# Kernel tuning notes

Hardware: AMD Instinct MI355X
Metric: run time of the kernel (lower is better)

The kernel has to match this reference:

```python
import jax, jax.numpy as jnp
import numpy as np

# PointPillars KITTI config (from init_kwargs)
VOXEL_SIZE = np.array([0.16, 0.16, 4.0], dtype=np.float32)
PC_LO = np.array([0.0, -39.68, -3.0], dtype=np.float32)
PC_HI = np.array([69.12, 39.68, 1.0], dtype=np.float32)
GRID = np.round((PC_HI - PC_LO) / VOXEL_SIZE).astype(np.int32)  # [432, 496, 1]
MAX_PTS = 32
MAX_VOX = 40000  # forward uses max_voxels[1]
B, N, C = 4, 120000, 4


def _voxelize_one(pts):
    """Hard-voxelize one point cloud. pts: (N, C) float32.
    Returns padded (MAX_VOX, MAX_PTS, C) voxels, (MAX_VOX, 3) int32 coords
    (x,y,z; -1 for padding slots), (MAX_VOX,) int32 point counts (0 = padding).
    Voxels are ordered by first occurrence in point order, and points within a
    voxel are filled in point order (first MAX_PTS), matching hard_voxelize_cpu."""
    grid = jnp.asarray(GRID)
    lo = jnp.asarray(PC_LO)
    hi = jnp.asarray(PC_HI)
    vs = jnp.asarray(VOXEL_SIZE)

    xyz = pts[:, :3]
    inb = jnp.all((xyz >= lo) & (xyz < hi), axis=1)                       # (N,)
    coords = jnp.clip(jnp.floor((xyz - lo) / vs).astype(jnp.int32), 0, grid - 1)
    flat = coords[:, 0] * (grid[1] * grid[2]) + coords[:, 1] * grid[2] + coords[:, 2]
    SENT = jnp.int32(int(GRID[0]) * int(GRID[1]) * int(GRID[2]))
    flat = jnp.where(inb, flat, SENT)                                     # out-of-range -> sentinel bin

    # stable sort groups equal flat-ids while preserving point order
    order_s = jnp.argsort(flat, stable=True)                              # (N,)
    fs = flat[order_s]
    is_first = jnp.concatenate([jnp.ones((1,), bool), fs[1:] != fs[:-1]])
    gid_s = jnp.cumsum(is_first.astype(jnp.int32)) - 1                    # group id per sorted pos

    # per-group stats (num_segments = N covers worst case; empty segs -> int max)
    first_pt = jax.ops.segment_min(order_s.astype(jnp.int32), gid_s, num_segments=N)
    group_flat = jax.ops.segment_min(fs, gid_s, num_segments=N)
    cnt_g = jax.ops.segment_sum(jnp.ones((N,), jnp.int32), gid_s, num_segments=N)
    valid_g = group_flat < SENT

    # slot = rank of first occurrence among valid groups (np.argsort(first_idx))
    key = jnp.where(valid_g, first_pt, jnp.int32(N))
    g_order = jnp.argsort(key)
    slot_of_group = jnp.zeros((N,), jnp.int32).at[g_order].set(jnp.arange(N, dtype=jnp.int32))

    # per-point group / slot / within-voxel rank (rank = order of arrival)
    pgid = jnp.zeros((N,), jnp.int32).at[order_s].set(gid_s)
    pslot = slot_of_group[pgid]
    start_s = jax.ops.segment_min(jnp.arange(N, dtype=jnp.int32), gid_s, num_segments=N)
    wrank_s = jnp.arange(N, dtype=jnp.int32) - start_s[gid_s]
    wrank = jnp.zeros((N,), jnp.int32).at[order_s].set(wrank_s)

    pvalid = inb & (pslot < MAX_VOX) & (wrank < MAX_PTS)
    tslot = jnp.where(pvalid, pslot, jnp.int32(MAX_VOX))                  # dump invalid into pad row
    trank = jnp.where(pvalid, wrank, 0)
    voxels = jnp.zeros((MAX_VOX + 1, MAX_PTS, C), pts.dtype).at[tslot, trank].set(pts)[:MAX_VOX]

    gslot = jnp.where(valid_g & (slot_of_group < MAX_VOX), slot_of_group, jnp.int32(MAX_VOX))
    gcoords = coords[jnp.clip(first_pt, 0, N - 1)]
    out_coords = jnp.full((MAX_VOX + 1, 3), -1, jnp.int32).at[gslot].set(gcoords)[:MAX_VOX]
    npts = jnp.zeros((MAX_VOX + 1,), jnp.int32).at[gslot].set(jnp.minimum(cnt_g, MAX_PTS))[:MAX_VOX]
    return voxels, out_coords, npts


def setup_inputs() -> dict:
    key = jax.random.key(0)
    k1, k2 = jax.random.split(key)
    # xyz uniform slightly beyond the pc_range so some points are filtered out
    lo = jnp.array([-2.0, -42.0, -3.2], jnp.float32)
    hi = jnp.array([71.0, 42.0, 1.2], jnp.float32)
    xyz = lo + jax.random.uniform(k1, (B, N, 3), jnp.float32) * (hi - lo)
    inten = jax.random.uniform(k2, (B, N, 1), jnp.float32)
    return {"points": jnp.concatenate([xyz, inten], axis=-1)}


def reference(points):
    voxels, coords, npts = jax.vmap(_voxelize_one)(points)                # (B, MAX_VOX, ...)
    pillars = voxels.reshape(B * MAX_VOX, MAX_PTS, C)
    batch_idx = jnp.broadcast_to(jnp.arange(B, dtype=jnp.int32)[:, None, None], (B, MAX_VOX, 1))
    # padding slots (npts == 0) keep batch idx -1 like their -1 coords
    batch_idx = jnp.where(npts[..., None] > 0, batch_idx, -1)
    coors_batch = jnp.concatenate([batch_idx, coords], axis=-1).reshape(B * MAX_VOX, 4)
    npoints = npts.reshape(B * MAX_VOX)
    return pillars, coors_batch, npoints
```

## Files before the change

### kernel.cpp

```cpp
#include <hip/hip_runtime.h>
#include <stdint.h>

#define BB      4
#define NPTS    120000
#define GX      432
#define GY      496
#define GG      (GX*GY)
#define MAXVOX  40000
#define MAXP    32
#define CHUNK   512
#define NCH     235
#define NBLK    (BB*NCH)
#define NT      (NBLK*256)

#define OFF_COOR 20480000
#define OFF_NPTS 21120000

#define POISON    0xAAAAAAAAu
#define SPIN_CAP  (1u<<22)
#define AGENT __HIP_MEMORY_SCOPE_AGENT


__device__ __forceinline__ unsigned aload(const unsigned* p) {
    return __hip_atomic_load(p, __ATOMIC_RELAXED, AGENT);
}
__device__ __forceinline__ void astore(unsigned* p, unsigned v) {
    __hip_atomic_store(p, v, __ATOMIC_RELAXED, AGENT);
}

__device__ __forceinline__ int compute_flat(float4 pt) {
    float x = pt.x, y = pt.y, z = pt.z;
    bool inb = (x >= 0.0f) && (x < 69.12f) &&
               (y >= -39.68f) && (y < 39.68f) &&
               (z >= -3.0f) && (z < 1.0f);
    if (!inb) return -1;
    int cx = (int)floorf((x - 0.0f) / 0.16f);
    int cy = (int)floorf((y + 39.68f) / 0.16f);
    cx = min(max(cx, 0), GX - 1);
    cy = min(max(cy, 0), GY - 1);
    return cx * GY + cy;
}

__global__ __launch_bounds__(256) void k1z(const float* __restrict__ pts,
        unsigned int* __restrict__ head, unsigned int* __restrict__ nxt,
        float* __restrict__ out)
{
    const int tid = threadIdx.x, blk = blockIdx.x;
    const int b = blk / NCH, c = blk - b * NCH;
    const int base = c * CHUNK;
    const float4* pp = (const float4*)pts + (size_t)b * NPTS;
    const int p0 = base + tid, p1 = base + 256 + tid;
    int f0 = -1, f1 = -1;
    if (p0 < NPTS) f0 = compute_flat(pp[p0]);
    if (p1 < NPTS) f1 = compute_flat(pp[p1]);
    if (f0 >= 0)
        nxt[b * NPTS + p0] = atomicExch(&head[b * GG + f0], (unsigned)p0);
    if (f1 >= 0)
        nxt[b * NPTS + p1] = atomicExch(&head[b * GG + f1], (unsigned)p1);

    const int gt = blk * 256 + tid;
    const float4 z = make_float4(0.f, 0.f, 0.f, 0.f);
    float4* o4 = (float4*)out;
    for (int i = gt; i < 5120000; i += NT) o4[i] = z;
    const float4 neg1 = make_float4(-1.f, -1.f, -1.f, -1.f);
    float4* c4 = (float4*)(out + OFF_COOR);
    if (gt < 160000) c4[gt] = neg1;
    float4* n4 = (float4*)(out + OFF_NPTS);
    if (gt < 40000) n4[gt] = z;
}

__global__ __launch_bounds__(256) void k2w(const float* __restrict__ pts,
        const unsigned int* __restrict__ head, const unsigned int* __restrict__ nxt,
        unsigned int* __restrict__ descr, float* __restrict__ out)
{
    const int tid = threadIdx.x, blk = blockIdx.x;
    const int b = blk / NCH, c = blk - b * NCH;
    const int base = c * CHUNK;
    const int lane = tid & 63, wv = tid >> 6;
    const int p0 = base + tid, p1 = base + 256 + tid;
    const float4* pp = (const float4*)pts + (size_t)b * NPTS;
    const unsigned* nx = nxt + (size_t)b * NPTS;

    int f0 = -1, f1 = -1;
    if (p0 < NPTS) f0 = compute_flat(pp[p0]);
    if (p1 < NPTS) f1 = compute_flat(pp[p1]);
    unsigned hd0 = 0, hd1 = 0, mn0 = 0xFFFFFFFFu, mn1 = 0xFFFFFFFFu;
    int cnt0 = 0, cnt1 = 0;
    if (f0 >= 0) {
        hd0 = head[b * GG + f0];
        for (unsigned node = hd0; node != POISON; node = nx[node]) {
            ++cnt0; mn0 = min(mn0, node);
        }
    }
    if (f1 >= 0) {
        hd1 = head[b * GG + f1];
        for (unsigned node = hd1; node != POISON; node = nx[node]) {
            ++cnt1; mn1 = min(mn1, node);
        }
    }
    int flag0 = (f0 >= 0 && mn0 == (unsigned)p0);
    int flag1 = (f1 >= 0 && mn1 == (unsigned)p1);

    unsigned long long mA = __ballot(flag0);
    unsigned long long mB = __ballot(flag1);
    __shared__ int wsA[4], wsB[4];
    __shared__ int s_excl;
    if (lane == 0) { wsA[wv] = __popcll(mA); wsB[wv] = __popcll(mB); }
    __syncthreads();
    int preA = 0, preB = 0, totA = 0, totB = 0;
    #pragma unroll
    for (int i = 0; i < 4; ++i) {
        if (i < wv) { preA += wsA[i]; preB += wsB[i]; }
        totA += wsA[i]; totB += wsB[i];
    }
    unsigned long long below = (1ull << lane) - 1ull;
    int rank0 = preA + __popcll(mA & below);
    int rank1 = totA + preB + __popcll(mB & below);
    int total = totA + totB;

    if (tid == 0 && c > 0)
        astore(&descr[blk], 0x40000000u | (unsigned)total);

    if (wv == 0) {
        int excl = 0, pos = c;
        while (pos > 0) {
            int w = min(64, pos);
            int st = 0, val = 0;
            if (lane < w) {
                const unsigned* src = &descr[b * NCH + (pos - 1 - lane)];
                unsigned word; unsigned it = 0;
                do { word = aload(src); st = (int)(word >> 30); }
                while (!(st & 1) && ++it < SPIN_CAP);
                val = (int)(word & 0x3FFFFFFFu);
            }
            unsigned long long pmask = __ballot(st == 3);
            int contrib;
            if (pmask) {
                int j = (int)(__ffsll((long long)pmask) - 1);
                contrib = (lane <= j) ? val : 0;
                pos = 0;
            } else {
                contrib = (lane < w) ? val : 0;
                pos -= w;
            }
            #pragma unroll
            for (int off = 1; off < 64; off <<= 1)
                contrib += __shfl_xor(contrib, off, 64);
            excl += contrib;
        }
        if (lane == 0) {
            s_excl = excl;
            astore(&descr[blk], 0xC0000000u | (unsigned)(excl + total));
        }
    }
    __syncthreads();
    int excl = s_excl;

    #pragma unroll
    for (int h = 0; h < 2; ++h) {
        int flg = h ? flag1 : flag0;
        if (!flg) continue;
        int f = h ? f1 : f0;
        int s = excl + (h ? rank1 : rank0);
        if (s >= MAXVOX) continue;
        unsigned hd = h ? hd1 : hd0;
        int cnt = h ? cnt1 : cnt0;
        int t = b * MAXVOX + s;
        int m = min(cnt, MAXP);
        float4* prow = (float4*)out + (size_t)t * MAXP;
        int prev = -1;
        for (int r = 0; r < m; ++r) {
            int cur = 0x7FFFFFFF;
            for (unsigned node = hd; node != POISON; node = nx[node]) {
                int pi = (int)node;
                if (pi > prev && pi < cur) cur = pi;
            }
            prow[r] = pp[cur];
            prev = cur;
        }
        float* coor = out + (size_t)OFF_COOR + (size_t)t * 4;
        coor[0] = (float)b;
        coor[1] = (float)(f / GY);
        coor[2] = (float)(f % GY);
        coor[3] = 0.f;
        out[OFF_NPTS + t] = (float)m;
    }
}

extern "C" void kernel_launch(void* const* d_in, const int* in_sizes, int n_in,
                              void* d_out, int out_size, void* d_ws, size_t ws_size,
                              hipStream_t stream) {
    const float* pts = (const float*)d_in[0];
    float* out = (float*)d_out;

    auto align256 = [](size_t x) { return (x + 255) & ~(size_t)255; };
    char* w = (char*)d_ws;
    unsigned int* head  = (unsigned int*)w; w += align256((size_t)BB * GG * 4);
    unsigned int* nxt   = (unsigned int*)w; w += align256((size_t)BB * NPTS * 4);
    unsigned int* descr = (unsigned int*)w; w += align256((size_t)NBLK * 4);

    k1z<<<NBLK, 256, 0, stream>>>(pts, head, nxt, out);
    k2w<<<NBLK, 256, 0, stream>>>(pts, head, nxt, descr, out);
}
```

Before: 136.9 us.

## Fuse linking and compaction kernels via cooperative grid sync, early-exit chain walk

```diff
diff --git a/kernel.cpp b/kernel.cpp
--- a/kernel.cpp
+++ b/kernel.cpp
@@ -1,4 +1,5 @@
 #include <hip/hip_runtime.h>
+#include <hip/hip_cooperative_groups.h>
 #include <stdint.h>
 
 #define BB      4
@@ -20,6 +21,8 @@
 #define SPIN_CAP  (1u<<22)
 #define AGENT __HIP_MEMORY_SCOPE_AGENT
 
+namespace cg = cooperative_groups;
+
 
 __device__ __forceinline__ unsigned aload(const unsigned* p) {
     return __hip_atomic_load(p, __ATOMIC_RELAXED, AGENT);
@@ -41,22 +44,25 @@
     return cx * GY + cy;
 }
 
-__global__ __launch_bounds__(256) void k1z(const float* __restrict__ pts,
+__global__ __launch_bounds__(256, 4) void kf(const float* __restrict__ pts,
         unsigned int* __restrict__ head, unsigned int* __restrict__ nxt,
-        float* __restrict__ out)
+        unsigned int* __restrict__ descr, float* __restrict__ out)
 {
     const int tid = threadIdx.x, blk = blockIdx.x;
     const int b = blk / NCH, c = blk - b * NCH;
     const int base = c * CHUNK;
+    const int lane = tid & 63, wv = tid >> 6;
+    const int p0 = base + tid, p1 = base + 256 + tid;
     const float4* pp = (const float4*)pts + (size_t)b * NPTS;
-    const int p0 = base + tid, p1 = base + 256 + tid;
+    unsigned* nx = nxt + (size_t)b * NPTS;
+
     int f0 = -1, f1 = -1;
     if (p0 < NPTS) f0 = compute_flat(pp[p0]);
     if (p1 < NPTS) f1 = compute_flat(pp[p1]);
     if (f0 >= 0)
-        nxt[b * NPTS + p0] = atomicExch(&head[b * GG + f0], (unsigned)p0);
+        nx[p0] = atomicExch(&head[b * GG + f0], (unsigned)p0);
     if (f1 >= 0)
-        nxt[b * NPTS + p1] = atomicExch(&head[b * GG + f1], (unsigned)p1);
+        nx[p1] = atomicExch(&head[b * GG + f1], (unsigned)p1);
 
     const int gt = blk * 256 + tid;
     const float4 z = make_float4(0.f, 0.f, 0.f, 0.f);
@@ -67,39 +73,30 @@
     if (gt < 160000) c4[gt] = neg1;
     float4* n4 = (float4*)(out + OFF_NPTS);
     if (gt < 40000) n4[gt] = z;
-}
-
-__global__ __launch_bounds__(256) void k2w(const float* __restrict__ pts,
-        const unsigned int* __restrict__ head, const unsigned int* __restrict__ nxt,
-        unsigned int* __restrict__ descr, float* __restrict__ out)
-{
-    const int tid = threadIdx.x, blk = blockIdx.x;
-    const int b = blk / NCH, c = blk - b * NCH;
-    const int base = c * CHUNK;
-    const int lane = tid & 63, wv = tid >> 6;
-    const int p0 = base + tid, p1 = base + 256 + tid;
-    const float4* pp = (const float4*)pts + (size_t)b * NPTS;
-    const unsigned* nx = nxt + (size_t)b * NPTS;
-
-    int f0 = -1, f1 = -1;
-    if (p0 < NPTS) f0 = compute_flat(pp[p0]);
-    if (p1 < NPTS) f1 = compute_flat(pp[p1]);
-    unsigned hd0 = 0, hd1 = 0, mn0 = 0xFFFFFFFFu, mn1 = 0xFFFFFFFFu;
+
+    __builtin_amdgcn_fence(__ATOMIC_RELEASE, "agent");
+    cg::this_grid().sync();
+    __builtin_amdgcn_fence(__ATOMIC_ACQUIRE, "agent");
+
+    unsigned hd0 = 0, hd1 = 0;
     int cnt0 = 0, cnt1 = 0;
+    int flag0 = 0, flag1 = 0;
     if (f0 >= 0) {
         hd0 = head[b * GG + f0];
+        flag0 = 1;
         for (unsigned node = hd0; node != POISON; node = nx[node]) {
-            ++cnt0; mn0 = min(mn0, node);
+            ++cnt0;
+            if ((int)node < p0) { flag0 = 0; break; }
         }
     }
     if (f1 >= 0) {
         hd1 = head[b * GG + f1];
+        flag1 = 1;
         for (unsigned node = hd1; node != POISON; node = nx[node]) {
-            ++cnt1; mn1 = min(mn1, node);
-        }
-    }
-    int flag0 = (f0 >= 0 && mn0 == (unsigned)p0);
-    int flag1 = (f1 >= 0 && mn1 == (unsigned)p1);
+            ++cnt1;
+            if ((int)node < p1) { flag1 = 0; break; }
+        }
+    }
 
     unsigned long long mA = __ballot(flag0);
     unsigned long long mB = __ballot(flag1);
@@ -187,6 +184,150 @@
     }
 }
 
+__global__ __launch_bounds__(256) void k1z(const float* __restrict__ pts,
+        unsigned int* __restrict__ head, unsigned int* __restrict__ nxt,
+        float* __restrict__ out)
+{
+    const int tid = threadIdx.x, blk = blockIdx.x;
+    const int b = blk / NCH, c = blk - b * NCH;
+    const int base = c * CHUNK;
+    const float4* pp = (const float4*)pts + (size_t)b * NPTS;
+    const int p0 = base + tid, p1 = base + 256 + tid;
+    int f0 = -1, f1 = -1;
+    if (p0 < NPTS) f0 = compute_flat(pp[p0]);
+    if (p1 < NPTS) f1 = compute_flat(pp[p1]);
+    if (f0 >= 0)
+        nxt[b * NPTS + p0] = atomicExch(&head[b * GG + f0], (unsigned)p0);
+    if (f1 >= 0)
+        nxt[b * NPTS + p1] = atomicExch(&head[b * GG + f1], (unsigned)p1);
+
+    const int gt = blk * 256 + tid;
+    const float4 z = make_float4(0.f, 0.f, 0.f, 0.f);
+    float4* o4 = (float4*)out;
+    for (int i = gt; i < 5120000; i += NT) o4[i] = z;
+    const float4 neg1 = make_float4(-1.f, -1.f, -1.f, -1.f);
+    float4* c4 = (float4*)(out + OFF_COOR);
+    if (gt < 160000) c4[gt] = neg1;
+    float4* n4 = (float4*)(out + OFF_NPTS);
+    if (gt < 40000) n4[gt] = z;
+}
+
+__global__ __launch_bounds__(256) void k2w(const float* __restrict__ pts,
+        const unsigned int* __restrict__ head, const unsigned int* __restrict__ nxt,
+        unsigned int* __restrict__ descr, float* __restrict__ out)
+{
+    const int tid = threadIdx.x, blk = blockIdx.x;
+    const int b = blk / NCH, c = blk - b * NCH;
+    const int base = c * CHUNK;
+    const int lane = tid & 63, wv = tid >> 6;
+    const int p0 = base + tid, p1 = base + 256 + tid;
+    const float4* pp = (const float4*)pts + (size_t)b * NPTS;
+    const unsigned* nx = nxt + (size_t)b * NPTS;
+
+    int f0 = -1, f1 = -1;
+    if (p0 < NPTS) f0 = compute_flat(pp[p0]);
+    if (p1 < NPTS) f1 = compute_flat(pp[p1]);
+    unsigned hd0 = 0, hd1 = 0;
+    int cnt0 = 0, cnt1 = 0, flag0 = 0, flag1 = 0;
+    if (f0 >= 0) {
+        hd0 = head[b * GG + f0]; flag0 = 1;
+        for (unsigned node = hd0; node != POISON; node = nx[node]) {
+            ++cnt0; if ((int)node < p0) { flag0 = 0; break; }
+        }
+    }
+    if (f1 >= 0) {
+        hd1 = head[b * GG + f1]; flag1 = 1;
+        for (unsigned node = hd1; node != POISON; node = nx[node]) {
+            ++cnt1; if ((int)node < p1) { flag1 = 0; break; }
+        }
+    }
+
+    unsigned long long mA = __ballot(flag0);
+    unsigned long long mB = __ballot(flag1);
+    __shared__ int wsA[4], wsB[4];
+    __shared__ int s_excl;
+    if (lane == 0) { wsA[wv] = __popcll(mA); wsB[wv] = __popcll(mB); }
+    __syncthreads();
+    int preA = 0, preB = 0, totA = 0, totB = 0;
+    #pragma unroll
+    for (int i = 0; i < 4; ++i) {
+        if (i < wv) { preA += wsA[i]; preB += wsB[i]; }
+        totA += wsA[i]; totB += wsB[i];
+    }
+    unsigned long long below = (1ull << lane) - 1ull;
+    int rank0 = preA + __popcll(mA & below);
+    int rank1 = totA + preB + __popcll(mB & below);
+    int total = totA + totB;
+
+    if (tid == 0 && c > 0)
+        astore(&descr[blk], 0x40000000u | (unsigned)total);
+
+    if (wv == 0) {
+        int excl = 0, pos = c;
+        while (pos > 0) {
+            int w = min(64, pos);
+            int st = 0, val = 0;
+            if (lane < w) {
+                const unsigned* src = &descr[b * NCH + (pos - 1 - lane)];
+                unsigned word; unsigned it = 0;
+                do { word = aload(src); st = (int)(word >> 30); }
+                while (!(st & 1) && ++it < SPIN_CAP);
+                val = (int)(word & 0x3FFFFFFFu);
+            }
+            unsigned long long pmask = __ballot(st == 3);
+            int contrib;
+            if (pmask) {
+                int j = (int)(__ffsll((long long)pmask) - 1);
+                contrib = (lane <= j) ? val : 0;
+                pos = 0;
+            } else {
+                contrib = (lane < w) ? val : 0;
+                pos -= w;
+            }
+            #pragma unroll
+            for (int off = 1; off < 64; off <<= 1)
+                contrib += __shfl_xor(contrib, off, 64);
+            excl += contrib;
+        }
+        if (lane == 0) {
+            s_excl = excl;
+            astore(&descr[blk], 0xC0000000u | (unsigned)(excl + total));
+        }
+    }
+    __syncthreads();
+    int excl = s_excl;
+
+    #pragma unroll
+    for (int h = 0; h < 2; ++h) {
+        int flg = h ? flag1 : flag0;
+        if (!flg) continue;
+        int f = h ? f1 : f0;
+        int s = excl + (h ? rank1 : rank0);
+        if (s >= MAXVOX) continue;
+        unsigned hd = h ? hd1 : hd0;
+        int cnt = h ? cnt1 : cnt0;
+        int t = b * MAXVOX + s;
+        int m = min(cnt, MAXP);
+        float4* prow = (float4*)out + (size_t)t * MAXP;
+        int prev = -1;
+        for (int r = 0; r < m; ++r) {
+            int cur = 0x7FFFFFFF;
+            for (unsigned node = hd; node != POISON; node = nx[node]) {
+                int pi = (int)node;
+                if (pi > prev && pi < cur) cur = pi;
+            }
+            prow[r] = pp[cur];
+            prev = cur;
+        }
+        float* coor = out + (size_t)OFF_COOR + (size_t)t * 4;
+        coor[0] = (float)b;
+        coor[1] = (float)(f / GY);
+        coor[2] = (float)(f % GY);
+        coor[3] = 0.f;
+        out[OFF_NPTS + t] = (float)m;
+    }
+}
+
 extern "C" void kernel_launch(void* const* d_in, const int* in_sizes, int n_in,
                               void* d_out, int out_size, void* d_ws, size_t ws_size,
                               hipStream_t stream) {
@@ -199,6 +340,12 @@
     unsigned int* nxt   = (unsigned int*)w; w += align256((size_t)BB * NPTS * 4);
     unsigned int* descr = (unsigned int*)w; w += align256((size_t)NBLK * 4);
 
-    k1z<<<NBLK, 256, 0, stream>>>(pts, head, nxt, out);
-    k2w<<<NBLK, 256, 0, stream>>>(pts, head, nxt, descr, out);
-}
+    void* args[] = { (void*)&pts, (void*)&head, (void*)&nxt,
+                     (void*)&descr, (void*)&out };
+    hipError_t e = hipLaunchCooperativeKernel(reinterpret_cast<void*>(kf),
+                       dim3(NBLK), dim3(256), args, 0, stream);
+    if (e != hipSuccess) {
+        k1z<<<NBLK, 256, 0, stream>>>(pts, head, nxt, out);
+        k2w<<<NBLK, 256, 0, stream>>>(pts, head, nxt, descr, out);
+    }
+}
```

Result: slower. 369.3 us (+169.7%).

## Drop full output zero-fill; pad only unused rows and tail slots

Applied to the files above, without the earlier changes.

```diff
diff --git a/kernel.cpp b/kernel.cpp
--- a/kernel.cpp
+++ b/kernel.cpp
@@ -21,6 +21,7 @@
 #define AGENT __HIP_MEMORY_SCOPE_AGENT
 
 
+
 __device__ __forceinline__ unsigned aload(const unsigned* p) {
     return __hip_atomic_load(p, __ATOMIC_RELAXED, AGENT);
 }
@@ -41,9 +42,8 @@
     return cx * GY + cy;
 }
 
-__global__ __launch_bounds__(256) void k1z(const float* __restrict__ pts,
-        unsigned int* __restrict__ head, unsigned int* __restrict__ nxt,
-        float* __restrict__ out)
+__global__ __launch_bounds__(256) void k1a(const float* __restrict__ pts,
+        unsigned int* __restrict__ head, unsigned int* __restrict__ nxt)
 {
     const int tid = threadIdx.x, blk = blockIdx.x;
     const int b = blk / NCH, c = blk - b * NCH;
@@ -57,19 +57,9 @@
         nxt[b * NPTS + p0] = atomicExch(&head[b * GG + f0], (unsigned)p0);
     if (f1 >= 0)
         nxt[b * NPTS + p1] = atomicExch(&head[b * GG + f1], (unsigned)p1);
-
-    const int gt = blk * 256 + tid;
-    const float4 z = make_float4(0.f, 0.f, 0.f, 0.f);
-    float4* o4 = (float4*)out;
-    for (int i = gt; i < 5120000; i += NT) o4[i] = z;
-    const float4 neg1 = make_float4(-1.f, -1.f, -1.f, -1.f);
-    float4* c4 = (float4*)(out + OFF_COOR);
-    if (gt < 160000) c4[gt] = neg1;
-    float4* n4 = (float4*)(out + OFF_NPTS);
-    if (gt < 40000) n4[gt] = z;
-}
-
-__global__ __launch_bounds__(256) void k2w(const float* __restrict__ pts,
+}
+
+__global__ __launch_bounds__(256) void k2e(const float* __restrict__ pts,
         const unsigned int* __restrict__ head, const unsigned int* __restrict__ nxt,
         unsigned int* __restrict__ descr, float* __restrict__ out)
 {
@@ -84,22 +74,20 @@
     int f0 = -1, f1 = -1;
     if (p0 < NPTS) f0 = compute_flat(pp[p0]);
     if (p1 < NPTS) f1 = compute_flat(pp[p1]);
-    unsigned hd0 = 0, hd1 = 0, mn0 = 0xFFFFFFFFu, mn1 = 0xFFFFFFFFu;
-    int cnt0 = 0, cnt1 = 0;
+    unsigned hd0 = 0, hd1 = 0;
+    int cnt0 = 0, cnt1 = 0, flag0 = 0, flag1 = 0;
     if (f0 >= 0) {
-        hd0 = head[b * GG + f0];
+        hd0 = head[b * GG + f0]; flag0 = 1;
         for (unsigned node = hd0; node != POISON; node = nx[node]) {
-            ++cnt0; mn0 = min(mn0, node);
+            ++cnt0; if ((int)node < p0) { flag0 = 0; break; }
         }
     }
     if (f1 >= 0) {
-        hd1 = head[b * GG + f1];
+        hd1 = head[b * GG + f1]; flag1 = 1;
         for (unsigned node = hd1; node != POISON; node = nx[node]) {
-            ++cnt1; mn1 = min(mn1, node);
-        }
-    }
-    int flag0 = (f0 >= 0 && mn0 == (unsigned)p0);
-    int flag1 = (f1 >= 0 && mn1 == (unsigned)p1);
+            ++cnt1; if ((int)node < p1) { flag1 = 0; break; }
+        }
+    }
 
     unsigned long long mA = __ballot(flag0);
     unsigned long long mB = __ballot(flag1);
@@ -156,6 +144,8 @@
     __syncthreads();
     int excl = s_excl;
 
+    const float4 z4 = make_float4(0.f, 0.f, 0.f, 0.f);
+
     #pragma unroll
     for (int h = 0; h < 2; ++h) {
         int flg = h ? flag1 : flag0;
@@ -178,6 +168,7 @@
             prow[r] = pp[cur];
             prev = cur;
         }
+        for (int r = m; r < MAXP; ++r) prow[r] = z4;
         float* coor = out + (size_t)OFF_COOR + (size_t)t * 4;
         coor[0] = (float)b;
         coor[1] = (float)(f / GY);
@@ -185,6 +176,18 @@
         coor[3] = 0.f;
         out[OFF_NPTS + t] = (float)m;
     }
+
+    if (c == NCH - 1) {
+        int T = excl + total;
+        const float4 n4 = make_float4(-1.f, -1.f, -1.f, -1.f);
+        for (int s = T + tid; s < MAXVOX; s += 256) {
+            int t = b * MAXVOX + s;
+            float4* prow = (float4*)out + (size_t)t * MAXP;
+            for (int r = 0; r < MAXP; ++r) prow[r] = z4;
+            ((float4*)(out + OFF_COOR))[t] = n4;
+            out[OFF_NPTS + t] = 0.f;
+        }
+    }
 }
 
 extern "C" void kernel_launch(void* const* d_in, const int* in_sizes, int n_in,
@@ -199,6 +202,6 @@
     unsigned int* nxt   = (unsigned int*)w; w += align256((size_t)BB * NPTS * 4);
     unsigned int* descr = (unsigned int*)w; w += align256((size_t)NBLK * 4);
 
-    k1z<<<NBLK, 256, 0, stream>>>(pts, head, nxt, out);
-    k2w<<<NBLK, 256, 0, stream>>>(pts, head, nxt, descr, out);
-}
+    k1a<<<NBLK, 256, 0, stream>>>(pts, head, nxt);
+    k2e<<<NBLK, 256, 0, stream>>>(pts, head, nxt, descr, out);
+}
```

Measured after the change: 158.4 us. 1.16x slower.

## Swizzle block-to-batch mapping across XCDs and early-exit first-point chain walk

Applied to the files above, without the earlier changes.

```diff
diff --git a/kernel.cpp b/kernel.cpp
--- a/kernel.cpp
+++ b/kernel.cpp
@@ -11,7 +11,8 @@
 #define CHUNK   512
 #define NCH     235
 #define NBLK    (BB*NCH)
-#define NT      (NBLK*256)
+#define NBLK_PAD 944
+#define NT_PAD  (NBLK_PAD*256)
 
 #define OFF_COOR 20480000
 #define OFF_NPTS 21120000
@@ -19,6 +20,7 @@
 #define POISON    0xAAAAAAAAu
 #define SPIN_CAP  (1u<<22)
 #define AGENT __HIP_MEMORY_SCOPE_AGENT
+
 
 
 __device__ __forceinline__ unsigned aload(const unsigned* p) {
@@ -41,27 +43,35 @@
     return cx * GY + cy;
 }
 
-__global__ __launch_bounds__(256) void k1z(const float* __restrict__ pts,
+__device__ __forceinline__ void swz_map(int g, int& b, int& c) {
+    int xcd = g & 7, slot = g >> 3;
+    b = xcd >> 1;
+    c = (slot << 1) | (xcd & 1);
+}
+
+__global__ __launch_bounds__(256) void k1s(const float* __restrict__ pts,
         unsigned int* __restrict__ head, unsigned int* __restrict__ nxt,
         float* __restrict__ out)
 {
-    const int tid = threadIdx.x, blk = blockIdx.x;
-    const int b = blk / NCH, c = blk - b * NCH;
-    const int base = c * CHUNK;
-    const float4* pp = (const float4*)pts + (size_t)b * NPTS;
-    const int p0 = base + tid, p1 = base + 256 + tid;
-    int f0 = -1, f1 = -1;
-    if (p0 < NPTS) f0 = compute_flat(pp[p0]);
-    if (p1 < NPTS) f1 = compute_flat(pp[p1]);
-    if (f0 >= 0)
-        nxt[b * NPTS + p0] = atomicExch(&head[b * GG + f0], (unsigned)p0);
-    if (f1 >= 0)
-        nxt[b * NPTS + p1] = atomicExch(&head[b * GG + f1], (unsigned)p1);
-
-    const int gt = blk * 256 + tid;
+    const int tid = threadIdx.x, g = blockIdx.x;
+    int b, c; swz_map(g, b, c);
+
+    if (c < NCH) {
+        const int base = c * CHUNK;
+        const int p0 = base + tid, p1 = base + 256 + tid;
+        const float4* pp = (const float4*)pts + (size_t)b * NPTS;
+        int f0 = (p0 < NPTS) ? compute_flat(pp[p0]) : -1;
+        int f1 = (p1 < NPTS) ? compute_flat(pp[p1]) : -1;
+        if (f0 >= 0)
+            nxt[b * NPTS + p0] = atomicExch(&head[b * GG + f0], (unsigned)p0);
+        if (f1 >= 0)
+            nxt[b * NPTS + p1] = atomicExch(&head[b * GG + f1], (unsigned)p1);
+    }
+
+    const int gt = g * 256 + tid;
     const float4 z = make_float4(0.f, 0.f, 0.f, 0.f);
     float4* o4 = (float4*)out;
-    for (int i = gt; i < 5120000; i += NT) o4[i] = z;
+    for (int i = gt; i < 5120000; i += NT_PAD) o4[i] = z;
     const float4 neg1 = make_float4(-1.f, -1.f, -1.f, -1.f);
     float4* c4 = (float4*)(out + OFF_COOR);
     if (gt < 160000) c4[gt] = neg1;
@@ -69,12 +79,13 @@
     if (gt < 40000) n4[gt] = z;
 }
 
-__global__ __launch_bounds__(256) void k2w(const float* __restrict__ pts,
+__global__ __launch_bounds__(256) void k2s(const float* __restrict__ pts,
         const unsigned int* __restrict__ head, const unsigned int* __restrict__ nxt,
         unsigned int* __restrict__ descr, float* __restrict__ out)
 {
-    const int tid = threadIdx.x, blk = blockIdx.x;
-    const int b = blk / NCH, c = blk - b * NCH;
+    const int tid = threadIdx.x, g = blockIdx.x;
+    int b, c; swz_map(g, b, c);
+    if (c >= NCH) return;
     const int base = c * CHUNK;
     const int lane = tid & 63, wv = tid >> 6;
     const int p0 = base + tid, p1 = base + 256 + tid;
@@ -84,22 +95,20 @@
     int f0 = -1, f1 = -1;
     if (p0 < NPTS) f0 = compute_flat(pp[p0]);
     if (p1 < NPTS) f1 = compute_flat(pp[p1]);
-    unsigned hd0 = 0, hd1 = 0, mn0 = 0xFFFFFFFFu, mn1 = 0xFFFFFFFFu;
-    int cnt0 = 0, cnt1 = 0;
+    unsigned hd0 = 0, hd1 = 0;
+    int cnt0 = 0, cnt1 = 0, flag0 = 0, flag1 = 0;
     if (f0 >= 0) {
-        hd0 = head[b * GG + f0];
+        hd0 = head[b * GG + f0]; flag0 = 1;
         for (unsigned node = hd0; node != POISON; node = nx[node]) {
-            ++cnt0; mn0 = min(mn0, node);
+            ++cnt0; if ((int)node < p0) { flag0 = 0; break; }
         }
     }
     if (f1 >= 0) {
-        hd1 = head[b * GG + f1];
+        hd1 = head[b * GG + f1]; flag1 = 1;
         for (unsigned node = hd1; node != POISON; node = nx[node]) {
-            ++cnt1; mn1 = min(mn1, node);
-        }
-    }
-    int flag0 = (f0 >= 0 && mn0 == (unsigned)p0);
-    int flag1 = (f1 >= 0 && mn1 == (unsigned)p1);
+            ++cnt1; if ((int)node < p1) { flag1 = 0; break; }
+        }
+    }
 
     unsigned long long mA = __ballot(flag0);
     unsigned long long mB = __ballot(flag1);
@@ -119,7 +128,7 @@
     int total = totA + totB;
 
     if (tid == 0 && c > 0)
-        astore(&descr[blk], 0x40000000u | (unsigned)total);
+        astore(&descr[b * NCH + c], 0x40000000u | (unsigned)total);
 
     if (wv == 0) {
         int excl = 0, pos = c;
@@ -150,7 +159,7 @@
         }
         if (lane == 0) {
             s_excl = excl;
-            astore(&descr[blk], 0xC0000000u | (unsigned)(excl + total));
+            astore(&descr[b * NCH + c], 0xC0000000u | (unsigned)(excl + total));
         }
     }
     __syncthreads();
@@ -199,6 +208,6 @@
     unsigned int* nxt   = (unsigned int*)w; w += align256((size_t)BB * NPTS * 4);
     unsigned int* descr = (unsigned int*)w; w += align256((size_t)NBLK * 4);
 
-    k1z<<<NBLK, 256, 0, stream>>>(pts, head, nxt, out);
-    k2w<<<NBLK, 256, 0, stream>>>(pts, head, nxt, descr, out);
-}
+    k1s<<<NBLK_PAD, 256, 0, stream>>>(pts, head, nxt, out);
+    k2s<<<NBLK_PAD, 256, 0, stream>>>(pts, head, nxt, descr, out);
+}
```

Measured after the change: 133.6 us. 2.5% less time.
